# Performance work log

Measured on AMD Instinct MI355X. Metric: run time of the kernel, lower is better.

## Reference

```python
import jax, jax.numpy as jnp
import numpy as np

B, S, D, A_DIM = 8, 2048, 256, 64

def setup_inputs() -> dict:
    key = jax.random.key(0)
    k_x, k_wm, k_wl, k_eps = jax.random.split(key, 4)
    return {
        "x": jax.random.normal(k_x, (B, S, D), dtype=jnp.float32),
        "W_mean": jax.random.normal(k_wm, (D, A_DIM), dtype=jnp.float32) * (1.0 / np.sqrt(D)),
        "b_mean": jnp.zeros((A_DIM,), dtype=jnp.float32),
        "W_logvar": jax.random.normal(k_wl, (D, A_DIM), dtype=jnp.float32) * (1.0 / np.sqrt(D)),
        "b_logvar": jnp.zeros((A_DIM,), dtype=jnp.float32),
        "eps": jax.random.normal(k_eps, (B, S, A_DIM), dtype=jnp.float32),
    }

def reference(x, W_mean, b_mean, W_logvar, b_logvar, eps):
    d = x.shape[-1]
    scale = 1.0 / jnp.sqrt(jnp.asarray(d, dtype=x.dtype))
    # S_det = x x^T / sqrt(d)  -> [B, S, S]
    scores = jnp.einsum("bsd,btd->bst", x, x) * scale
    attn = jax.nn.softmax(scores, axis=-1)
    # A_det = softmax(S) x  -> [B, S, D]
    A_det = jnp.einsum("bst,btd->bsd", attn, x)
    A_mean = A_det @ W_mean + b_mean        # [B, S, A_DIM]
    A_logvar = A_det @ W_logvar + b_logvar  # [B, S, A_DIM]
    A = A_mean + jnp.exp(0.5 * A_logvar) * eps  # sqrt(exp(logvar)) = exp(logvar/2)
    return (A_mean, A_logvar, A)
```

## Files before the change

### kernel.cpp

```cpp
#include <hip/hip_runtime.h>

#define B_ 8
#define S_ 2048
#define D_ 256

typedef _Float16 f16;
typedef f16 f16x2 __attribute__((ext_vector_type(2)));
typedef f16 f16x8 __attribute__((ext_vector_type(8)));
typedef float f32x16 __attribute__((ext_vector_type(16)));
typedef unsigned int u32;
typedef u32 u32x4 __attribute__((ext_vector_type(4)));

typedef const __attribute__((address_space(1))) unsigned int* gptr_t;
typedef __attribute__((address_space(3))) unsigned int* lptr_t;

__device__ __forceinline__ void gload_lds16(const void* g, void* l) {
  __builtin_amdgcn_global_load_lds((gptr_t)(unsigned long long)g,
                                   (lptr_t)(unsigned long long)l, 16, 0, 0);
}

__device__ __forceinline__ u32 packf16(float a, float b) {
  f16x2 t; t[0] = (f16)a; t[1] = (f16)b;
  return __builtin_bit_cast(u32, t);
}

__device__ __forceinline__ void pack16(const f32x16& p, int hi, u32x4& o0, u32x4& o1) {
#pragma unroll
  for (int c2 = 0; c2 < 2; ++c2) {
    u32 a1 = packf16(p[8 * c2 + 0], p[8 * c2 + 1]);
    u32 a2 = packf16(p[8 * c2 + 2], p[8 * c2 + 3]);
    u32 b1 = packf16(p[8 * c2 + 4], p[8 * c2 + 5]);
    u32 b2 = packf16(p[8 * c2 + 6], p[8 * c2 + 7]);
    u32 xa1 = __shfl_xor(a1, 32), xa2 = __shfl_xor(a2, 32);
    u32 xb1 = __shfl_xor(b1, 32), xb2 = __shfl_xor(b2, 32);
    u32x4 f;
    f[0] = hi ? xb1 : a1;
    f[1] = hi ? xb2 : a2;
    f[2] = hi ? b1 : xa1;
    f[3] = hi ? b2 : xa2;
    if (c2) o1 = f; else o0 = f;
  }
}

#define SC2F 0.09016844f
#define NMAXR 20.0f
#define SWZ(r, s) ((s) ^ ((r) & 3) ^ (((r) >> 2) & 3))

__global__ void prep(const float* __restrict__ x, const float* __restrict__ Wm,
                     const float* __restrict__ Wl, f16* __restrict__ xh,
                     f16* __restrict__ xt, float* __restrict__ n2,
                     f16* __restrict__ Wt) {
  __shared__ f16 tile[64][264];
  const int bid = blockIdx.x;
  const int t = threadIdx.x;
  if (bid < 256) {
    const int b = bid >> 5, st = bid & 31;
    const int s0 = st * 64;
    const float* xb = x + ((size_t)(b * S_ + s0)) * D_;
    f16* xhb = xh + ((size_t)(b * S_ + s0)) * D_;
#pragma unroll
    for (int it = 0; it < 16; ++it) {
      int flat = it * 256 + t;
      int r = flat >> 6, c4 = flat & 63;
      float4 v = *reinterpret_cast<const float4*>(xb + r * 256 + c4 * 4);
      f16 h0 = (f16)v.x, h1 = (f16)v.y, h2 = (f16)v.z, h3 = (f16)v.w;
      f16x2 p0 = {h0, h1}, p1 = {h2, h3};
      uint2 wv; wv.x = __builtin_bit_cast(u32, p0); wv.y = __builtin_bit_cast(u32, p1);
      *reinterpret_cast<uint2*>(xhb + r * 256 + c4 * 4) = wv;
      tile[r][c4 * 4 + 0] = h0; tile[r][c4 * 4 + 1] = h1;
      tile[r][c4 * 4 + 2] = h2; tile[r][c4 * 4 + 3] = h3;
    }
    __syncthreads();
    {
      int r = t >> 2, qd = t & 3;
      float s = 0.0f;
#pragma unroll
      for (int i = 0; i < 8; ++i) {
        f16x8 v = *reinterpret_cast<const f16x8*>(&tile[r][qd * 64 + i * 8]);
#pragma unroll
        for (int u = 0; u < 8; ++u) { float f = (float)v[u]; s += f * f; }
      }
      s += __shfl_xor(s, 1); s += __shfl_xor(s, 2);
      if (qd == 0) n2[b * S_ + s0 + r] = s;
    }
    {
      f16* xtb = xt + ((size_t)(b * D_ + t)) * S_ + s0;
#pragma unroll
      for (int s8 = 0; s8 < 8; ++s8) {
        f16x8 ov;
#pragma unroll
        for (int u = 0; u < 8; ++u) ov[u] = tile[s8 * 8 + u][t];
        *reinterpret_cast<f16x8*>(xtb + s8 * 8) = ov;
      }
    }
  } else {
    int idx = (bid - 256) * 1024 + t * 4;
    int j = idx >> 8, d = idx & 255;
#pragma unroll
    for (int k2 = 0; k2 < 4; ++k2) {
      float v = (j < 64) ? Wm[(d + k2) * 64 + j] : Wl[(d + k2) * 64 + (j - 64)];
      Wt[idx + k2] = (f16)v;
    }
  }
}

__launch_bounds__(512, 4)
__global__ void gemm1_kern(const f16* __restrict__ xh, const float* __restrict__ n2,
                           f16* __restrict__ P, float* __restrict__ Lp,
                           int b0, int bm, int bsh) {
  __shared__ __align__(16) char smem[65536];
  f16* Aq = (f16*)smem;
  f16* Bk = (f16*)(smem + 32768);
  const int idx = blockIdx.x;
  const int bl = idx & bm;
  int tdec = idx >> bsh;
  int qt = 0;
#pragma unroll 1
  while (tdec >= 16 - qt) { tdec -= 16 - qt; ++qt; }
  const int kt = qt + tdec;
  const int b = b0 + bl;
  const int qb = qt * 128, kb = kt * 128;
  const int tid = threadIdx.x, lane = tid & 63, w = tid >> 6;
  const int l31 = lane & 31, hi = lane >> 5;
  const int wq = w >> 2, wk = w & 3;
  const f16* xb = xh + (size_t)b * S_ * D_;

#define G1_STAGE(st, pp)                                                       \
  { _Pragma("unroll") for (int i = 0; i < 4; ++i) {                            \
      int ii = w * 4 + i;                                                      \
      int flat = ii * 64 + lane;                                               \
      bool isB = ii >= 16;                                                     \
      int ch = isB ? flat - 1024 : flat;                                       \
      int r = ch >> 3, c = ch & 7;                                             \
      int csrc = c ^ (r & 7);                                                  \
      const f16* src = xb + (size_t)((isB ? kb : qb) + r) * 256 +              \
                       (st) * 64 + csrc * 8;                                   \
      f16* dst = (isB ? Bk : Aq) + ((pp) * 8192) + ch * 8;                     \
      gload_lds16(src, dst);                                                   \
    } }

  f32x16 acc[2];
#pragma unroll
  for (int i = 0; i < 2; ++i)
#pragma unroll
    for (int e = 0; e < 16; ++e) acc[i][e] = 0.0f;

  G1_STAGE(0, 0);
  __syncthreads();
#pragma unroll
  for (int t = 0; t < 4; ++t) {
    const int p = t & 1;
    if (t < 3) G1_STAGE(t + 1, p ^ 1);
#pragma unroll
    for (int kc = 0; kc < 4; ++kc) {
      int cc = ((2 * kc + hi) ^ (l31 & 7)) * 8;
      f16x8 af  = *reinterpret_cast<const f16x8*>(Bk + p * 8192 + (wk * 32 + l31) * 64 + cc);
      f16x8 bf0 = *reinterpret_cast<const f16x8*>(Aq + p * 8192 + (wq * 64 + l31) * 64 + cc);
      f16x8 bf1 = *reinterpret_cast<const f16x8*>(Aq + p * 8192 + (wq * 64 + 32 + l31) * 64 + cc);
      acc[0] = __builtin_amdgcn_mfma_f32_32x32x16_f16(af, bf0, acc[0], 0, 0, 0);
      acc[1] = __builtin_amdgcn_mfma_f32_32x32x16_f16(af, bf1, acc[1], 0, 0, 0);
    }
    __syncthreads();
  }
#undef G1_STAGE

  float* raw = (float*)smem;
  if (kt != qt) {
#pragma unroll
    for (int ni = 0; ni < 2; ++ni)
#pragma unroll
      for (int j = 0; j < 16; ++j) {
        int kvloc = wk * 32 + (j & 3) + 8 * (j >> 2) + 4 * hi;
        int qloc = wq * 64 + ni * 32 + l31;
        raw[kvloc * 128 + (qloc ^ ((kvloc & 7) << 2))] = acc[ni][j];
      }
  }

  float r2[2], lsum[2];
  int qrow[2];
#pragma unroll
  for (int ni = 0; ni < 2; ++ni) {
    qrow[ni] = qb + wq * 64 + ni * 32 + l31;
    r2[ni] = sqrtf(n2[b * S_ + qrow[ni]]) * (NMAXR * SC2F);
    lsum[ni] = 0.0f;
  }
#pragma unroll
  for (int ni = 0; ni < 2; ++ni)
#pragma unroll
    for (int j = 0; j < 16; ++j) {
      float v = exp2f(acc[ni][j] * SC2F - r2[ni]);
      acc[ni][j] = v;
      lsum[ni] += v;
    }
#pragma unroll
  for (int ni = 0; ni < 2; ++ni) lsum[ni] += __shfl_xor(lsum[ni], 32);

  const int colb = kb + wk * 32;
#pragma unroll
  for (int ni = 0; ni < 2; ++ni) {
    u32x4 s0, s1;
    pack16(acc[ni], hi, s0, s1);
    size_t rowp = (size_t)(bl * S_ + qrow[ni]) * 2048;
    *reinterpret_cast<u32x4*>(P + rowp + colb + hi * 8) = s0;
    *reinterpret_cast<u32x4*>(P + rowp + colb + 16 + hi * 8) = s1;
  }

  if (kt != qt) {
    __syncthreads();
    const int kvr = tid >> 2;
    const int qseg = (tid & 3) * 32;
    float r2kv = sqrtf(n2[b * S_ + kb + kvr]) * (NMAXR * SC2F);
    u32 ow[16];
    float tsum = 0.0f;
#pragma unroll
    for (int c8 = 0; c8 < 8; ++c8) {
      int qs = qseg + c8 * 4;
      float4 v = *reinterpret_cast<const float4*>(
          &raw[kvr * 128 + (qs ^ ((kvr & 7) << 2))]);
      float e0 = exp2f(v.x * SC2F - r2kv), e1 = exp2f(v.y * SC2F - r2kv);
      float e2 = exp2f(v.z * SC2F - r2kv), e3 = exp2f(v.w * SC2F - r2kv);
      tsum += (e0 + e1) + (e2 + e3);
      ow[c8 * 2 + 0] = packf16(e0, e1);
      ow[c8 * 2 + 1] = packf16(e2, e3);
    }
    size_t rowp = (size_t)(bl * S_ + kb + kvr) * 2048;
#pragma unroll
    for (int sseg = 0; sseg < 4; ++sseg) {
      u32x4 sv;
      sv[0] = ow[sseg * 4 + 0]; sv[1] = ow[sseg * 4 + 1];
      sv[2] = ow[sseg * 4 + 2]; sv[3] = ow[sseg * 4 + 3];
      *reinterpret_cast<u32x4*>(P + rowp + qb + qseg + sseg * 8) = sv;
    }
    tsum += __shfl_xor(tsum, 1);
    tsum += __shfl_xor(tsum, 2);
    if ((tid & 3) == 0)
      Lp[(size_t)(bl * 16 + qt) * 2048 + kb + kvr] = tsum;
  }

  __syncthreads();
  float* Lred = (float*)smem;
  if (hi == 0) {
    Lred[(wq * 64 + l31) * 4 + wk] = lsum[0];
    Lred[(wq * 64 + 32 + l31) * 4 + wk] = lsum[1];
  }
  __syncthreads();
  if (tid < 128) {
    float s = Lred[tid * 4] + Lred[tid * 4 + 1] + Lred[tid * 4 + 2] + Lred[tid * 4 + 3];
    Lp[(size_t)(bl * 16 + kt) * 2048 + qb + tid] = s;
  }
}

__launch_bounds__(512, 6)
__global__ void gemm2_kern(const f16* __restrict__ P, const f16* __restrict__ xt,
                           const float* __restrict__ Lp, f16* __restrict__ adet,
                           int b0, int bm, int bsh) {
  __shared__ f16 Pt[2][8192];
  __shared__ f16 Xt[2][4096];
  const int idx = blockIdx.x;
  const int bl = idx & bm;
  const int dt = (idx >> bsh) & 3;
  const int qt = idx >> (bsh + 2);
  const int b = b0 + bl;
  const int qb = qt * 128, db = dt * 64;
  const int tid = threadIdx.x, lane = tid & 63, w = tid >> 6;
  const int l31 = lane & 31, hi = lane >> 5;
  const int wq = w >> 1, wd = w & 1;
  const f16* xtb = xt + (size_t)b * D_ * S_;

#define G2_STAGE(st, pp)                                                       \
  { _Pragma("unroll") for (int i = 0; i < 3; ++i) {                            \
      int ii = w * 3 + i;                                                      \
      int flat = ii * 64 + lane;                                               \
      bool isX = ii >= 16;                                                     \
      int ch = isX ? flat - 1024 : flat;                                       \
      int r = ch >> 3, c = ch & 7;                                             \
      int csrc = c ^ (r & 7);                                                  \
      const f16* src = isX                                                     \
          ? xtb + (size_t)(db + r) * 2048 + ((st) * 64) + csrc * 8             \
          : P + (size_t)(bl * S_ + qb + r) * 2048 + ((st) * 64) + csrc * 8;    \
      f16* dst = (isX ? &Xt[(pp)][0] : &Pt[(pp)][0]) + ch * 8;                 \
      gload_lds16(src, dst);                                                   \
    } }

  f32x16 acc;
#pragma unroll
  for (int e = 0; e < 16; ++e) acc[e] = 0.0f;

  G2_STAGE(0, 0);
  __syncthreads();
#pragma unroll 1
  for (int t = 0; t < 32; ++t) {
    const int p = t & 1;
    if (t < 31) G2_STAGE(t + 1, p ^ 1);
#pragma unroll
    for (int kc = 0; kc < 4; ++kc) {
      int cc = ((2 * kc + hi) ^ (l31 & 7)) * 8;
      f16x8 af = *reinterpret_cast<const f16x8*>(&Xt[p][(wd * 32 + l31) * 64 + cc]);
      f16x8 bf = *reinterpret_cast<const f16x8*>(&Pt[p][(wq * 32 + l31) * 64 + cc]);
      acc = __builtin_amdgcn_mfma_f32_32x32x16_f16(af, bf, acc, 0, 0, 0);
    }
    __syncthreads();
  }
#undef G2_STAGE

  const int q = qb + wq * 32 + l31;
  float L = 0.0f;
#pragma unroll
  for (int kt = 0; kt < 16; ++kt) L += Lp[(size_t)(bl * 16 + kt) * 2048 + q];
  float rL = 1.0f / L;
#pragma unroll
  for (int e = 0; e < 16; ++e) acc[e] *= rL;
  u32x4 s0, s1;
  pack16(acc, hi, s0, s1);
  f16* arow = adet + (size_t)(b * S_ + q) * 256 + db + wd * 32;
  *reinterpret_cast<u32x4*>(arow + hi * 8) = s0;
  *reinterpret_cast<u32x4*>(arow + 16 + hi * 8) = s1;
}

__launch_bounds__(64)
__global__ void proj_kern(const f16* __restrict__ adet, const f16* __restrict__ Wt,
                          const float* __restrict__ bm, const float* __restrict__ bl,
                          const float* __restrict__ eps, float* __restrict__ out) {
  const int lane = threadIdx.x & 63;
  const int l31 = lane & 31, hi = lane >> 5;
  const int bidx = blockIdx.x;
  const int rb = ((bidx & 7) * 64 + (bidx >> 3)) * 32;
  f16x8 af[16];
  const f16* arow = adet + (size_t)(rb + l31) * 256;
#pragma unroll
  for (int kk = 0; kk < 16; ++kk)
    af[kk] = *reinterpret_cast<const f16x8*>(arow + kk * 16 + hi * 8);
  f32x16 acc[4];
#pragma unroll
  for (int i = 0; i < 4; ++i)
#pragma unroll
    for (int j = 0; j < 16; ++j) acc[i][j] = 0.0f;
#pragma unroll
  for (int ns = 0; ns < 4; ++ns) {
    const f16* wrow = Wt + (size_t)(l31 + 32 * ns) * 256;
#pragma unroll
    for (int kk = 0; kk < 16; ++kk) {
      f16x8 bf = *reinterpret_cast<const f16x8*>(wrow + kk * 16 + hi * 8);
      acc[ns] = __builtin_amdgcn_mfma_f32_32x32x16_f16(af[kk], bf, acc[ns], 0, 0, 0);
    }
  }
#pragma unroll
  for (int ns = 0; ns < 2; ++ns) {
    int c = l31 + 32 * ns;
    float bmv = bm[c], blv = bl[c];
#pragma unroll
    for (int r = 0; r < 16; ++r) {
      int row = (r & 3) + 8 * (r >> 2) + 4 * hi;
      int grow = rb + row;
      float mean = acc[ns][r] + bmv;
      float lv = acc[ns + 2][r] + blv;
      float e = eps[grow * 64 + c];
      float a = mean + exp2f(0.7213475204f * lv) * e;
      out[grow * 64 + c] = mean;
      out[1048576 + grow * 64 + c] = lv;
      out[2097152 + grow * 64 + c] = a;
    }
  }
}

extern "C" void kernel_launch(void* const* d_in, const int* in_sizes, int n_in,
                              void* d_out, int out_size, void* d_ws, size_t ws_size,
                              hipStream_t stream) {
  (void)in_sizes; (void)n_in; (void)out_size;
  const float* x   = (const float*)d_in[0];
  const float* Wm  = (const float*)d_in[1];
  const float* bmv = (const float*)d_in[2];
  const float* Wl  = (const float*)d_in[3];
  const float* blv = (const float*)d_in[4];
  const float* ep  = (const float*)d_in[5];
  float* out = (float*)d_out;

  char* ws = (char*)d_ws;
  f16*   xh   = (f16*)(ws + 0);
  f16*   xt   = (f16*)(ws + 8388608);
  f16*   adet = (f16*)(ws + 16777216);
  f16*   Wt   = (f16*)(ws + 25165824);
  float* n2   = (float*)(ws + 25231360);
  float* Lp   = (float*)(ws + 25296896);
  const size_t P_off = 26345472;
  f16*   Pbuf = (f16*)(ws + P_off);

  int bpp = 1;
  if      (ws_size >= P_off + (size_t)8 * 2048 * 2048 * 2) bpp = 8;
  else if (ws_size >= P_off + (size_t)4 * 2048 * 2048 * 2) bpp = 4;
  else if (ws_size >= P_off + (size_t)2 * 2048 * 2048 * 2) bpp = 2;
  const int bsh = (bpp == 8) ? 3 : (bpp == 4) ? 2 : (bpp == 2) ? 1 : 0;
  const int bm = bpp - 1;

  prep<<<288, 256, 0, stream>>>(x, Wm, Wl, xh, xt, n2, Wt);
  for (int b0 = 0; b0 < 8; b0 += bpp) {
    gemm1_kern<<<bpp * 136, 512, 0, stream>>>(xh, n2, Pbuf, Lp, b0, bm, bsh);
    gemm2_kern<<<bpp * 64, 512, 0, stream>>>(Pbuf, xt, Lp, adet, b0, bm, bsh);
  }
  proj_kern<<<512, 64, 0, stream>>>(adet, Wt, bmv, blv, ep, out);
}
```

Measured before the change: 83.55 us.

## Reassociate attention output projection: precompute xW and fuse projection epilogue

Uses (softmax·x)·W = softmax·(x·W): a new kernel computes x·[W_mean|W_logvar] once per batch as a transposed fp16 buffer. The second GEMM then contracts P against this 128-wide product instead of the 256-wide x. It applies the softmax normalization, bias, exp and eps directly in its epilogue. This removes the x transpose in prep, the A_det intermediate buffer and the separate projection kernel, and halves the second GEMM's N dimension. The cost is an extra small GEMM launch and a coarser grid for the main second GEMM, which may hurt occupancy and latency hiding.

```diff
diff --git a/kernel.cpp b/kernel.cpp
--- a/kernel.cpp
+++ b/kernel.cpp
@@ -44,12 +44,10 @@
 
 #define SC2F 0.09016844f
 #define NMAXR 20.0f
-#define SWZ(r, s) ((s) ^ ((r) & 3) ^ (((r) >> 2) & 3))
 
 __global__ void prep(const float* __restrict__ x, const float* __restrict__ Wm,
                      const float* __restrict__ Wl, f16* __restrict__ xh,
-                     f16* __restrict__ xt, float* __restrict__ n2,
-                     f16* __restrict__ Wt) {
+                     float* __restrict__ n2, f16* __restrict__ Wt) {
   __shared__ f16 tile[64][264];
   const int bid = blockIdx.x;
   const int t = threadIdx.x;
@@ -83,16 +81,6 @@
       s += __shfl_xor(s, 1); s += __shfl_xor(s, 2);
       if (qd == 0) n2[b * S_ + s0 + r] = s;
     }
-    {
-      f16* xtb = xt + ((size_t)(b * D_ + t)) * S_ + s0;
-#pragma unroll
-      for (int s8 = 0; s8 < 8; ++s8) {
-        f16x8 ov;
-#pragma unroll
-        for (int u = 0; u < 8; ++u) ov[u] = tile[s8 * 8 + u][t];
-        *reinterpret_cast<f16x8*>(xtb + s8 * 8) = ov;
-      }
-    }
   } else {
     int idx = (bid - 256) * 1024 + t * 4;
     int j = idx >> 8, d = idx & 255;
@@ -101,6 +89,71 @@
       float v = (j < 64) ? Wm[(d + k2) * 64 + j] : Wl[(d + k2) * 64 + (j - 64)];
       Wt[idx + k2] = (f16)v;
     }
+  }
+}
+
+__launch_bounds__(256)
+__global__ void xw_kern(const f16* __restrict__ xh, const f16* __restrict__ Wt,
+                        f16* __restrict__ XWt) {
+  __shared__ f16 Ax[2][4096];
+  __shared__ f16 Ww[2][8192];
+  const int idx = blockIdx.x;
+  const int b = idx & 7;
+  const int sb = (idx >> 3) * 64;
+  const int tid = threadIdx.x, lane = tid & 63, w = tid >> 6;
+  const int l31 = lane & 31, hi = lane >> 5;
+  const f16* xb = xh + (size_t)b * S_ * D_;
+
+#define XW_STAGE(st, pp)                                                       \
+  {                                                                            \
+    _Pragma("unroll") for (int i = 0; i < 2; ++i) {                            \
+      int ch = i * 256 + tid; int r = ch >> 3, c = ch & 7;                     \
+      int csrc = c ^ (r & 7);                                                  \
+      gload_lds16(xb + (size_t)(sb + r) * 256 + ((st) * 64) + csrc * 8,        \
+                  &Ax[(pp)][0] + ch * 8);                                      \
+    }                                                                          \
+    _Pragma("unroll") for (int i = 0; i < 4; ++i) {                            \
+      int ch = i * 256 + tid; int r = ch >> 3, c = ch & 7;                     \
+      int csrc = c ^ (r & 7);                                                  \
+      gload_lds16(Wt + (size_t)r * 256 + ((st) * 64) + csrc * 8,               \
+                  &Ww[(pp)][0] + ch * 8);                                      \
+    }                                                                          \
+  }
+
+  f32x16 acc[2];
+#pragma unroll
+  for (int i = 0; i < 2; ++i)
+#pragma unroll
+    for (int e = 0; e < 16; ++e) acc[i][e] = 0.0f;
+
+  XW_STAGE(0, 0);
+  __syncthreads();
+#pragma unroll
+  for (int t = 0; t < 4; ++t) {
+    const int p = t & 1;
+    if (t < 3) XW_STAGE(t + 1, p ^ 1);
+#pragma unroll
+    for (int kc = 0; kc < 4; ++kc) {
+      int cc = ((2 * kc + hi) ^ (l31 & 7)) * 8;
+      f16x8 bf = *reinterpret_cast<const f16x8*>(&Ww[p][(w * 32 + l31) * 64 + cc]);
+#pragma unroll
+      for (int mi = 0; mi < 2; ++mi) {
+        f16x8 af = *reinterpret_cast<const f16x8*>(&Ax[p][(mi * 32 + l31) * 64 + cc]);
+        acc[mi] = __builtin_amdgcn_mfma_f32_32x32x16_f16(af, bf, acc[mi], 0, 0, 0);
+      }
+    }
+    __syncthreads();
+  }
+#undef XW_STAGE
+
+  const int j = w * 32 + l31;
+  f16* dst = XWt + ((size_t)b * 128 + j) * 2048;
+#pragma unroll
+  for (int mi = 0; mi < 2; ++mi) {
+    u32x4 s0, s1;
+    pack16(acc[mi], hi, s0, s1);
+    *reinterpret_cast<u32x4*>(dst + sb + mi * 32 + hi * 8) = s0;
+    *reinterpret_cast<u32x4*>(dst + sb + mi * 32 + 16 + hi * 8) = s1;
   }
 }
 
@@ -250,116 +303,94 @@
   }
 }
 
-__launch_bounds__(512, 6)
-__global__ void gemm2_kern(const f16* __restrict__ P, const f16* __restrict__ xt,
-                           const float* __restrict__ Lp, f16* __restrict__ adet,
-                           int b0, int bm, int bsh) {
-  __shared__ f16 Pt[2][8192];
-  __shared__ f16 Xt[2][4096];
+__launch_bounds__(256, 3)
+__global__ void gemm2p_kern(const f16* __restrict__ P, const f16* __restrict__ XWt,
+                            const float* __restrict__ Lp, const float* __restrict__ bm,
+                            const float* __restrict__ bl_, const float* __restrict__ eps,
+                            float* __restrict__ out, int b0, int bm_, int bsh) {
+  __shared__ f16 Pq[2][4096];
+  __shared__ f16 Xw[2][8192];
   const int idx = blockIdx.x;
-  const int bl = idx & bm;
-  const int dt = (idx >> bsh) & 3;
-  const int qt = idx >> (bsh + 2);
+  const int bl = idx & bm_;
+  const int qt = idx >> bsh;
   const int b = b0 + bl;
-  const int qb = qt * 128, db = dt * 64;
+  const int qb = qt * 64;
   const int tid = threadIdx.x, lane = tid & 63, w = tid >> 6;
   const int l31 = lane & 31, hi = lane >> 5;
-  const int wq = w >> 1, wd = w & 1;
-  const f16* xtb = xt + (size_t)b * D_ * S_;
-
-#define G2_STAGE(st, pp)                                                       \
-  { _Pragma("unroll") for (int i = 0; i < 3; ++i) {                            \
-      int ii = w * 3 + i;                                                      \
-      int flat = ii * 64 + lane;                                               \
-      bool isX = ii >= 16;                                                     \
-      int ch = isX ? flat - 1024 : flat;                                       \
-      int r = ch >> 3, c = ch & 7;                                             \
+  const int wq = w & 1, wc = w >> 1;
+  const f16* xwb = XWt + (size_t)b * 128 * 2048;
+
+#define GP_STAGE(tt, pp)                                                       \
+  {                                                                            \
+    _Pragma("unroll") for (int i = 0; i < 2; ++i) {                            \
+      int ch = i * 256 + tid; int r = ch >> 3, c = ch & 7;                     \
       int csrc = c ^ (r & 7);                                                  \
-      const f16* src = isX                                                     \
-          ? xtb + (size_t)(db + r) * 2048 + ((st) * 64) + csrc * 8             \
-          : P + (size_t)(bl * S_ + qb + r) * 2048 + ((st) * 64) + csrc * 8;    \
-      f16* dst = (isX ? &Xt[(pp)][0] : &Pt[(pp)][0]) + ch * 8;                 \
-      gload_lds16(src, dst);                                                   \
-    } }
-
-  f32x16 acc;
-#pragma unroll
-  for (int e = 0; e < 16; ++e) acc[e] = 0.0f;
-
-  G2_STAGE(0, 0);
+      gload_lds16(P + (size_t)(bl * S_ + qb + r) * 2048 + ((tt) * 64) + csrc * 8, \
+                  &Pq[(pp)][0] + ch * 8);                                      \
+    }                                                                          \
+    _Pragma("unroll") for (int i = 0; i < 4; ++i) {                            \
+      int ch = i * 256 + tid; int r = ch >> 3, c = ch & 7;                     \
+      int csrc = c ^ (r & 7);                                                  \
+      gload_lds16(xwb + (size_t)r * 2048 + ((tt) * 64) + csrc * 8,             \
+                  &Xw[(pp)][0] + ch * 8);                                      \
+    }                                                                          \
+  }
+
+  f32x16 acc[2];
+#pragma unroll
+  for (int i = 0; i < 2; ++i)
+#pragma unroll
+    for (int e = 0; e < 16; ++e) acc[i][e] = 0.0f;
+
+  GP_STAGE(0, 0);
   __syncthreads();
 #pragma unroll 1
   for (int t = 0; t < 32; ++t) {
     const int p = t & 1;
-    if (t < 31) G2_STAGE(t + 1, p ^ 1);
+    if (t < 31) GP_STAGE(t + 1, p ^ 1);
 #pragma unroll
     for (int kc = 0; kc < 4; ++kc) {
       int cc = ((2 * kc + hi) ^ (l31 & 7)) * 8;
-      f16x8 af = *reinterpret_cast<const f16x8*>(&Xt[p][(wd * 32 + l31) * 64 + cc]);
-      f16x8 bf = *reinterpret_cast<const f16x8*>(&Pt[p][(wq * 32 + l31) * 64 + cc]);
-      acc = __builtin_amdgcn_mfma_f32_32x32x16_f16(af, bf, acc, 0, 0, 0);
+      f16x8 bf = *reinterpret_cast<const f16x8*>(&Pq[p][(wq * 32 + l31) * 64 + cc]);
+#pragma unroll
+      for (int mi = 0; mi < 2; ++mi) {
+        int jrow = mi * 64 + wc * 32 + l31;
+        f16x8 af = *reinterpret_cast<const f16x8*>(&Xw[p][jrow * 64 + cc]);
+        acc[mi] = __builtin_amdgcn_mfma_f32_32x32x16_f16(af, bf, acc[mi], 0, 0, 0);
+      }
     }
     __syncthreads();
   }
-#undef G2_STAGE
+#undef GP_STAGE
 
   const int q = qb + wq * 32 + l31;
+  const int grow = b * S_ + q;
   float L = 0.0f;
 #pragma unroll
   for (int kt = 0; kt < 16; ++kt) L += Lp[(size_t)(bl * 16 + kt) * 2048 + q];
   float rL = 1.0f / L;
 #pragma unroll
-  for (int e = 0; e < 16; ++e) acc[e] *= rL;
-  u32x4 s0, s1;
-  pack16(acc, hi, s0, s1);
-  f16* arow = adet + (size_t)(b * S_ + q) * 256 + db + wd * 32;
-  *reinterpret_cast<u32x4*>(arow + hi * 8) = s0;
-  *reinterpret_cast<u32x4*>(arow + 16 + hi * 8) = s1;
-}
-
-__launch_bounds__(64)
-__global__ void proj_kern(const f16* __restrict__ adet, const f16* __restrict__ Wt,
-                          const float* __restrict__ bm, const float* __restrict__ bl,
-                          const float* __restrict__ eps, float* __restrict__ out) {
-  const int lane = threadIdx.x & 63;
-  const int l31 = lane & 31, hi = lane >> 5;
-  const int bidx = blockIdx.x;
-  const int rb = ((bidx & 7) * 64 + (bidx >> 3)) * 32;
-  f16x8 af[16];
-  const f16* arow = adet + (size_t)(rb + l31) * 256;
-#pragma unroll
-  for (int kk = 0; kk < 16; ++kk)
-    af[kk] = *reinterpret_cast<const f16x8*>(arow + kk * 16 + hi * 8);
-  f32x16 acc[4];
-#pragma unroll
-  for (int i = 0; i < 4; ++i)
-#pragma unroll
-    for (int j = 0; j < 16; ++j) acc[i][j] = 0.0f;
-#pragma unroll
-  for (int ns = 0; ns < 4; ++ns) {
-    const f16* wrow = Wt + (size_t)(l31 + 32 * ns) * 256;
-#pragma unroll
-    for (int kk = 0; kk < 16; ++kk) {
-      f16x8 bf = *reinterpret_cast<const f16x8*>(wrow + kk * 16 + hi * 8);
-      acc[ns] = __builtin_amdgcn_mfma_f32_32x32x16_f16(af[kk], bf, acc[ns], 0, 0, 0);
-    }
-  }
-#pragma unroll
-  for (int ns = 0; ns < 2; ++ns) {
-    int c = l31 + 32 * ns;
-    float bmv = bm[c], blv = bl[c];
-#pragma unroll
-    for (int r = 0; r < 16; ++r) {
-      int row = (r & 3) + 8 * (r >> 2) + 4 * hi;
-      int grow = rb + row;
-      float mean = acc[ns][r] + bmv;
-      float lv = acc[ns + 2][r] + blv;
-      float e = eps[grow * 64 + c];
-      float a = mean + exp2f(0.7213475204f * lv) * e;
-      out[grow * 64 + c] = mean;
-      out[1048576 + grow * 64 + c] = lv;
-      out[2097152 + grow * 64 + c] = a;
-    }
+  for (int jg = 0; jg < 4; ++jg) {
+    int cb = wc * 32 + 8 * jg + 4 * hi;
+    float4 bmv = *reinterpret_cast<const float4*>(bm + cb);
+    float4 blv = *reinterpret_cast<const float4*>(bl_ + cb);
+    float4 ev  = *reinterpret_cast<const float4*>(eps + (size_t)grow * 64 + cb);
+    float4 mn, lv, av;
+    float* mnp = &mn.x; float* lvp = &lv.x; float* avp = &av.x;
+    const float* bmp = &bmv.x; const float* blp = &blv.x; const float* evp = &ev.x;
+#pragma unroll
+    for (int jj = 0; jj < 4; ++jj) {
+      int j = jg * 4 + jj;
+      float m = acc[0][j] * rL + bmp[jj];
+      float l = acc[1][j] * rL + blp[jj];
+      mnp[jj] = m;
+      lvp[jj] = l;
+      avp[jj] = m + exp2f(0.7213475204f * l) * evp[jj];
+    }
+    float* o0 = out + (size_t)grow * 64 + cb;
+    *reinterpret_cast<float4*>(o0) = mn;
+    *reinterpret_cast<float4*>(o0 + 1048576) = lv;
+    *reinterpret_cast<float4*>(o0 + 2097152) = av;
   }
 }
 
@@ -377,12 +408,11 @@
 
   char* ws = (char*)d_ws;
   f16*   xh   = (f16*)(ws + 0);
-  f16*   xt   = (f16*)(ws + 8388608);
-  f16*   adet = (f16*)(ws + 16777216);
-  f16*   Wt   = (f16*)(ws + 25165824);
-  float* n2   = (float*)(ws + 25231360);
-  float* Lp   = (float*)(ws + 25296896);
-  const size_t P_off = 26345472;
+  f16*   XWt  = (f16*)(ws + 8388608);
+  f16*   Wt   = (f16*)(ws + 12582912);
+  float* n2   = (float*)(ws + 12648448);
+  float* Lp   = (float*)(ws + 12713984);
+  const size_t P_off = 13762560;
   f16*   Pbuf = (f16*)(ws + P_off);
 
   int bpp = 1;
@@ -392,10 +422,12 @@
   const int bsh = (bpp == 8) ? 3 : (bpp == 4) ? 2 : (bpp == 2) ? 1 : 0;
   const int bm = bpp - 1;
 
-  prep<<<288, 256, 0, stream>>>(x, Wm, Wl, xh, xt, n2, Wt);
+  prep<<<288, 256, 0, stream>>>(x, Wm, Wl, xh, n2, Wt);
+  xw_kern<<<256, 256, 0, stream>>>(xh, Wt, XWt);
   for (int b0 = 0; b0 < 8; b0 += bpp) {
     gemm1_kern<<<bpp * 136, 512, 0, stream>>>(xh, n2, Pbuf, Lp, b0, bm, bsh);
-    gemm2_kern<<<bpp * 64, 512, 0, stream>>>(Pbuf, xt, Lp, adet, b0, bm, bsh);
-  }
-  proj_kern<<<512, 64, 0, stream>>>(adet, Wt, bmv, blv, ep, out);
-}
+    gemm2p_kern<<<bpp * 32, 256, 0, stream>>>(Pbuf, XWt, Lp, bmv, blv, ep, out,
+                                              b0, bm, bsh);
+  }
+  proj_dummy:;
+}
```

New measurement: 75.90 us. 1.1x faster.
